# Kernel optimization log

Measured on AMD Instinct MI355X. Metric: run time of the kernel, lower is better.

Reference implementation:

```python
import jax, jax.numpy as jnp
import numpy as np

B, L, H, NH, D, I = 2, 2048, 2048, 16, 128, 8192
EPS = 1e-6
ROPE_BASE = 10000.0


def rms_norm(x, w):
    x32 = x.astype(jnp.float32)
    n = x32 * jax.lax.rsqrt(jnp.mean(x32 * x32, axis=-1, keepdims=True) + EPS)
    return (n * w).astype(x.dtype)


def rope(x, offset):
    # x: [B, L, H, D], non-traditional (half-split) RoPE
    d = x.shape[-1]
    half = d // 2
    inv_freq = 1.0 / (ROPE_BASE ** (jnp.arange(half, dtype=jnp.float32) * 2.0 / d))
    pos = jnp.arange(x.shape[1], dtype=jnp.float32) + offset
    ang = pos[:, None] * inv_freq[None, :]              # [L, half]
    cos = jnp.cos(ang)[None, :, None, :]
    sin = jnp.sin(ang)[None, :, None, :]
    x1, x2 = x[..., :half], x[..., half:]
    out = jnp.concatenate([x1 * cos - x2 * sin, x2 * cos + x1 * sin], axis=-1)
    return out.astype(x.dtype)


def setup_inputs() -> dict:
    key = jax.random.key(0)
    ks = jax.random.split(key, 9)
    s = 0.02
    causal = jnp.where(jnp.tril(jnp.ones((L, L), dtype=bool)), 0.0, -1e9).astype(jnp.float32)
    return {
        "x": jax.random.normal(ks[0], (B, L, H), dtype=jnp.float32),
        "ln1_w": jnp.ones((H,), dtype=jnp.float32),
        "ln2_w": jnp.ones((H,), dtype=jnp.float32),
        "wq": jax.random.normal(ks[1], (H, H), dtype=jnp.float32) * s,
        "wk": jax.random.normal(ks[2], (H, H), dtype=jnp.float32) * s,
        "wv": jax.random.normal(ks[3], (H, H), dtype=jnp.float32) * s,
        "wo": jax.random.normal(ks[4], (H, H), dtype=jnp.float32) * s,
        "w_gate": jax.random.normal(ks[5], (I, H), dtype=jnp.float32) * s,
        "w_up": jax.random.normal(ks[6], (I, H), dtype=jnp.float32) * s,
        "w_down": jax.random.normal(ks[7], (H, I), dtype=jnp.float32) * s,
        "mask": causal,
        "offset": 0,
    }


def reference(x, ln1_w, ln2_w, wq, wk, wv, wo, w_gate, w_up, w_down, mask, offset):
    residual = x
    h = rms_norm(x, ln1_w)
    # QKV projections (torch Linear: y = x @ W.T)
    q = jnp.einsum("ble,oe->blo", h, wq).reshape(B, L, NH, D)
    k = jnp.einsum("ble,oe->blo", h, wk).reshape(B, L, NH, D)
    v = jnp.einsum("ble,oe->blo", h, wv).reshape(B, L, NH, D)
    q = rope(q, offset)
    k = rope(k, offset)
    # [B, NH, L, D]
    q = q.transpose(0, 2, 1, 3)
    k = k.transpose(0, 2, 1, 3)
    v = v.transpose(0, 2, 1, 3)
    scores = jnp.einsum("bhqd,bhkd->bhqk", q.astype(jnp.float32), k.astype(jnp.float32))
    scores = scores / np.sqrt(D).astype(np.float32)
    if mask is not None:
        scores = scores + mask
    probs = jax.nn.softmax(scores, axis=-1).astype(v.dtype)
    attn = jnp.einsum("bhqk,bhkd->bhqd", probs, v)
    attn = attn.transpose(0, 2, 1, 3).reshape(B, L, NH * D)
    h = jnp.einsum("blo,eo->ble", attn, wo)
    x = h + residual
    residual = x
    h = rms_norm(x, ln2_w)
    gate = jax.nn.silu(jnp.einsum("ble,ie->bli", h, w_gate))
    up = jnp.einsum("ble,ie->bli", h, w_up)
    mlp = jnp.einsum("bli,ei->ble", gate * up, w_down)
    return mlp + residual
```

## Files before the change

### kernel.cpp

```cpp
#include <hip/hip_runtime.h>
#include <stdint.h>

#define B_ 2
#define L_ 2048
#define H_ 2048
#define NH_ 16
#define D_ 128
#define I_ 8192
#define M_ (B_*L_)

typedef unsigned short u16;
typedef __attribute__((ext_vector_type(8))) short bf16x8;
typedef __attribute__((ext_vector_type(4))) float f32x4;

__device__ __forceinline__ u16 f2bf(float f) {
  union { float f; uint32_t u; } c; c.f = f;
  return (u16)((c.u + 0x7fffu + ((c.u >> 16) & 1u)) >> 16);
}
__device__ __forceinline__ float bf2f(u16 h) {
  union { uint32_t u; float f; } c; c.u = ((uint32_t)h) << 16;
  return c.f;
}
__device__ __forceinline__ void gload16(const void* g, void* l) {
  __builtin_amdgcn_global_load_lds(
      (__attribute__((address_space(1))) void*)g,
      (__attribute__((address_space(3))) void*)l, 16, 0, 0);
}

__global__ void cvt_w(const float* __restrict__ src, u16* __restrict__ dst, int n4) {
  int i = blockIdx.x * blockDim.x + threadIdx.x;
  if (i >= n4) return;
  float4 v = ((const float4*)src)[i];
  ushort4 o;
  o.x = f2bf(v.x); o.y = f2bf(v.y); o.z = f2bf(v.z); o.w = f2bf(v.w);
  ((ushort4*)dst)[i] = o;
}

__global__ __launch_bounds__(256) void down_reduce(const u16* __restrict__ p0,
                                                   const u16* __restrict__ p1,
                                                   const float* __restrict__ res,
                                                   float* __restrict__ out, int n4) {
  int i = blockIdx.x * blockDim.x + threadIdx.x;
  if (i >= n4) return;
  ushort4 a = ((const ushort4*)p0)[i];
  ushort4 b = ((const ushort4*)p1)[i];
  float4 r = ((const float4*)res)[i];
  float4 o;
  o.x = bf2f(a.x) + bf2f(b.x) + r.x;
  o.y = bf2f(a.y) + bf2f(b.y) + r.y;
  o.z = bf2f(a.z) + bf2f(b.z) + r.z;
  o.w = bf2f(a.w) + bf2f(b.w) + r.w;
  ((float4*)out)[i] = o;
}

__global__ __launch_bounds__(256) void rmsnorm_k(const float* __restrict__ x,
                                                 const float* __restrict__ w,
                                                 u16* __restrict__ out) {
  int row = blockIdx.x;
  int t = threadIdx.x;
  const float4* xr = (const float4*)(x + (size_t)row * H_);
  float4 a = xr[t * 2], b = xr[t * 2 + 1];
  float s = a.x*a.x + a.y*a.y + a.z*a.z + a.w*a.w
          + b.x*b.x + b.y*b.y + b.z*b.z + b.w*b.w;
  for (int m = 1; m < 64; m <<= 1) s += __shfl_xor(s, m);
  __shared__ float sm[4];
  if ((t & 63) == 0) sm[t >> 6] = s;
  __syncthreads();
  float tot = sm[0] + sm[1] + sm[2] + sm[3];
  float rs = rsqrtf(tot / (float)H_ + 1e-6f);
  const float4* wr = (const float4*)w;
  float4 w0 = wr[t * 2], w1 = wr[t * 2 + 1];
  ushort4 o0, o1;
  o0.x = f2bf(a.x * rs * w0.x); o0.y = f2bf(a.y * rs * w0.y);
  o0.z = f2bf(a.z * rs * w0.z); o0.w = f2bf(a.w * rs * w0.w);
  o1.x = f2bf(b.x * rs * w1.x); o1.y = f2bf(b.y * rs * w1.y);
  o1.z = f2bf(b.z * rs * w1.z); o1.w = f2bf(b.w * rs * w1.w);
  ushort4* orow = (ushort4*)(out + (size_t)row * H_);
  orow[t * 2] = o0; orow[t * 2 + 1] = o1;
}

__global__ void rope_tab(float* __restrict__ cosT, float* __restrict__ sinT,
                         const int* __restrict__ offp) {
  int i = blockIdx.x * blockDim.x + threadIdx.x;
  int d = i & 63, l = i >> 6;
  float inv = powf(10000.0f, -(float)d / 64.0f);
  float ang = (float)(l + *offp) * inv;
  cosT[i] = cosf(ang);
  sinT[i] = sinf(ang);
}

__global__ void rope_apply(u16* __restrict__ qk, const float* __restrict__ cosT,
                           const float* __restrict__ sinT) {
  int i = blockIdx.x * blockDim.x + threadIdx.x;
  int d = i & 63;
  size_t row = (size_t)(i >> 6);
  int l = (int)(row & (L_ - 1));
  u16* p = qk + row * D_;
  float x1 = bf2f(p[d]), x2 = bf2f(p[d + 64]);
  float c = cosT[l * 64 + d], s = sinT[l * 64 + d];
  p[d]      = f2bf(x1 * c - x2 * s);
  p[d + 64] = f2bf(x2 * c + x1 * s);
}

__global__ __launch_bounds__(256) void vtrans_k(const u16* __restrict__ v,
                                                u16* __restrict__ vt) {
  __shared__ u16 tile[64][65];
  int l0 = blockIdx.x * 64, d0 = blockIdx.y * 64;
  size_t base = (size_t)blockIdx.z * L_ * D_;
  int t = threadIdx.x;
  int tr = t >> 3, tc = (t & 7) * 8;
  #pragma unroll
  for (int it = 0; it < 2; ++it) {
    int r = tr + it * 32;
    const u16* src = v + base + (size_t)(l0 + r) * D_ + d0 + tc;
    ushort4 u0 = ((const ushort4*)src)[0], u1 = ((const ushort4*)src)[1];
    tile[r][tc + 0] = u0.x; tile[r][tc + 1] = u0.y;
    tile[r][tc + 2] = u0.z; tile[r][tc + 3] = u0.w;
    tile[r][tc + 4] = u1.x; tile[r][tc + 5] = u1.y;
    tile[r][tc + 6] = u1.z; tile[r][tc + 7] = u1.w;
  }
  __syncthreads();
  #pragma unroll
  for (int it = 0; it < 2; ++it) {
    int r = tr + it * 32;
    u16* dst = vt + base + (size_t)(d0 + r) * L_ + l0 + tc;
    ushort4 o0, o1;
    o0.x = tile[tc + 0][r]; o0.y = tile[tc + 1][r];
    o0.z = tile[tc + 2][r]; o0.w = tile[tc + 3][r];
    o1.x = tile[tc + 4][r]; o1.y = tile[tc + 5][r];
    o1.z = tile[tc + 6][r]; o1.w = tile[tc + 7][r];
    ((ushort4*)dst)[0] = o0; ((ushort4*)dst)[1] = o1;
  }
}

#define EPI_SILU 1
#define EPI_MUL 2
#define EPI_PART 4
#define EPI_QKV3 5
#define EPI_GLU 6

template <int EPI>
__global__ __launch_bounds__(512, 2)
void gemm256(const u16* __restrict__ A, const u16* __restrict__ Bw,
             int M, int N, int K, int nk,
             u16* __restrict__ outb, u16* __restrict__ outb2,
             const u16* __restrict__ Bw2) {
  __shared__ __attribute__((aligned(16))) u16 Asm[2][2][8192];
  __shared__ __attribute__((aligned(16))) u16 Bsm[2][2][8192];
  int tid = threadIdx.x;
  int wid = tid >> 6, lane = tid & 63;
  int r16 = lane & 15, g4 = lane >> 4;
  int nwg = gridDim.x, bid = blockIdx.x;
  int q8 = nwg >> 3, r8 = nwg & 7, xcd = bid & 7, loc = bid >> 3;
  int wgall = (xcd < r8 ? xcd * (q8 + 1) : r8 * (q8 + 1) + (xcd - r8) * q8) + loc;
  int nwg_geo = (M >> 8) * ((EPI == EPI_GLU) ? (N >> 7) : (N >> 8));
  int ks = wgall / nwg_geo;
  int wg = wgall % nwg_geo;
  int MX = M >> 8;
  int m0 = (wg % MX) * 256;
  int n0 = (wg / MX) * ((EPI == EPI_GLU) ? 128 : 256);
  const char* Ab = (const char*)(A + (size_t)ks * nk * 64);
  const char* Bb = (const char*)(Bw + (size_t)ks * nk * 64);
  const char* Bb2 = (const char*)Bw2;
  u16* ob = (EPI == EPI_PART && ks) ? outb2 : outb;

  f32x4 acc[2][2][4][2] = {};
  bf16x8 afr[4][2];
  bf16x8 bfr[2][2][2];

  auto STAGE = [&](int kt1, int sel) {
    if (kt1 >= nk) return;
    int buf = kt1 & 1;
    int k0 = kt1 << 6;
    const char* gb; char* lb; int row0;
    if (sel == 0)      { gb = Ab; row0 = m0;       lb = (char*)&Asm[buf][0][0]; }
    else if (sel == 3) { gb = Ab; row0 = m0 + 128; lb = (char*)&Asm[buf][1][0]; }
    else if (sel == 1) { gb = Bb; row0 = n0;       lb = (char*)&Bsm[buf][0][0]; }
    else               { gb = (EPI == EPI_GLU) ? Bb2 : Bb;
                         row0 = (EPI == EPI_GLU) ? n0 : n0 + 128;
                         lb = (char*)&Bsm[buf][1][0]; }
    #pragma unroll
    for (int j = 0; j < 2; ++j) {
      int p = j * 8192 + wid * 1024 + lane * 16;
      int r = p >> 7;
      int cb = (p & 127) ^ ((r & 7) << 4);
      gload16(gb + ((size_t)(row0 + r) * K + k0) * 2 + cb,
              lb + j * 8192 + wid * 1024);
    }
  };

  STAGE(0, 0); STAGE(0, 1); STAGE(0, 2); STAGE(0, 3);

  const int QM[4] = {0, 0, 1, 1};
  const int QN[4] = {0, 1, 1, 0};

  for (int kt = 0; kt < nk; ++kt) {
    int cur = kt & 1;
    #pragma unroll
    for (int ph = 0; ph < 4; ++ph) {
      if (ph < 3) {
        __builtin_amdgcn_sched_barrier(0);
        asm volatile("s_waitcnt vmcnt(4)" ::: "memory");
      }
      __builtin_amdgcn_s_barrier();
      __builtin_amdgcn_sched_barrier(0);
      const int qm = QM[ph], qn = QN[ph];
      if (ph == 0 || ph == 2) {
        const char* Ah = (const char*)&Asm[cur][qm][0];
        #pragma unroll
        for (int mf = 0; mf < 4; ++mf) {
          int R = (wid >> 2) * 64 + mf * 16 + r16;
          int sw = (R & 7) << 4;
          afr[mf][0] = *(const bf16x8*)(Ah + R * 128 + ((g4 * 16) ^ sw));
          afr[mf][1] = *(const bf16x8*)(Ah + R * 128 + ((64 + g4 * 16) ^ sw));
        }
      }
      if (ph == 0 || ph == 1) {
        const char* Bh = (const char*)&Bsm[cur][qn][0];
        #pragma unroll
        for (int nf = 0; nf < 2; ++nf) {
          int R = (wid & 3) * 32 + nf * 16 + r16;
          int sw = (R & 7) << 4;
          bfr[qn][nf][0] = *(const bf16x8*)(Bh + R * 128 + ((g4 * 16) ^ sw));
          bfr[qn][nf][1] = *(const bf16x8*)(Bh + R * 128 + ((64 + g4 * 16) ^ sw));
        }
      }
      STAGE(kt + 1, ph);
      __builtin_amdgcn_s_setprio(1);
      #pragma unroll
      for (int mf = 0; mf < 4; ++mf)
        #pragma unroll
        for (int nf = 0; nf < 2; ++nf)
          #pragma unroll
          for (int kk = 0; kk < 2; ++kk)
            acc[qm][qn][mf][nf] = __builtin_amdgcn_mfma_f32_16x16x32_bf16(
                afr[mf][kk], bfr[qn][nf][kk], acc[qm][qn][mf][nf], 0, 0, 0);
      __builtin_amdgcn_s_setprio(0);
    }
  }
  if (EPI == EPI_GLU) {
    #pragma unroll
    for (int qm = 0; qm < 2; ++qm)
      #pragma unroll
      for (int mf = 0; mf < 4; ++mf)
        #pragma unroll
        for (int nf = 0; nf < 2; ++nf)
          #pragma unroll
          for (int rr = 0; rr < 4; ++rr) {
            int row = m0 + qm * 128 + (wid >> 2) * 64 + mf * 16 + g4 * 4 + rr;
            int col = n0 + (wid & 3) * 32 + nf * 16 + r16;
            float g = acc[qm][0][mf][nf][rr];
            float u = acc[qm][1][mf][nf][rr];
            float sg = g / (1.0f + __expf(-g));
            outb[(size_t)row * N + col] = f2bf(sg * u);
          }
    return;
  }
  #pragma unroll
  for (int qm = 0; qm < 2; ++qm)
    #pragma unroll
    for (int qn = 0; qn < 2; ++qn)
      #pragma unroll
      for (int mf = 0; mf < 4; ++mf)
        #pragma unroll
        for (int nf = 0; nf < 2; ++nf)
          #pragma unroll
          for (int rr = 0; rr < 4; ++rr) {
            int row = m0 + qm * 128 + (wid >> 2) * 64 + mf * 16 + g4 * 4 + rr;
            int col = n0 + qn * 128 + (wid & 3) * 32 + nf * 16 + r16;
            float val = acc[qm][qn][mf][nf][rr];
            if (EPI == EPI_SILU) {
              ob[(size_t)row * N + col] = f2bf(val / (1.0f + __expf(-val)));
            } else if (EPI == EPI_MUL) {
              float g = bf2f(ob[(size_t)row * N + col]);
              ob[(size_t)row * N + col] = f2bf(g * val);
            } else if (EPI == EPI_PART) {
              ob[(size_t)row * N + col] = f2bf(val);
            } else if (EPI == EPI_QKV3) {
              int which = col >> 11, within = col & 2047;
              int hh = within >> 7, d = within & 127;
              int bb = row >> 11, l = row & 2047;
              ob[(size_t)which * M_ * H_ +
                 ((((size_t)bb * NH_ + hh) * L_ + l) << 7) + d] = f2bf(val);
            }
          }
}

__global__ __launch_bounds__(256)
void flash_attn(const u16* __restrict__ q, const u16* __restrict__ k,
                const u16* __restrict__ vt, u16* __restrict__ out) {
  __shared__ __attribute__((aligned(16))) u16 Kt[2][64 * 128];
  __shared__ __attribute__((aligned(16))) u16 Vt[2][128 * 64];
  __shared__ __attribute__((aligned(16))) u16 Pl[4][16 * 64];
  int tid = threadIdx.x, w = tid >> 6, lane = tid & 63;
  int r16 = lane & 15, g4 = lane >> 4;
  int b = blockIdx.z, h = blockIdx.y;
  int qt = gridDim.x - 1 - blockIdx.x;
  int q0 = qt * 64;
  size_t bh = (size_t)b * NH_ + h;
  const char* qb = (const char*)(q + bh * L_ * D_);
  const char* kb = (const char*)(k + bh * L_ * D_);
  const char* vb = (const char*)(vt + bh * D_ * L_);
  int qrow = q0 + w * 16 + r16;
  bf16x8 qf[4];
  #pragma unroll
  for (int c = 0; c < 4; ++c)
    qf[c] = *(const bf16x8*)(qb + ((size_t)qrow * 128 + c * 32 + g4 * 8) * 2);
  f32x4 oacc[8] = {};
  float mrow[4], lsum[4];
  #pragma unroll
  for (int r = 0; r < 4; ++r) { mrow[r] = -3.0e38f; lsum[r] = 0.f; }
  int myq = q0 + w * 16 + g4 * 4;
  int ntiles = qt + 1;
  int rsw = (r16 & 7) << 4;
  const float sc = 0.08838834764831845f;

  auto STAGEKV = [&](int t, int buf) {
    if (t >= ntiles) return;
    int kv0 = t * 64;
    #pragma unroll
    for (int i = 0; i < 4; ++i) {
      int uoff = i * 4096 + w * 1024;
      int lin = uoff + lane * 16;
      int krow = lin >> 8;
      int kcol = (lin & 255) ^ ((krow & 7) << 4);
      gload16(kb + (size_t)(kv0 + krow) * 256 + kcol,
              (char*)&Kt[buf][0] + uoff);
      int vrow = lin >> 7;
      int vcol = (lin & 127) ^ ((vrow & 7) << 4);
      gload16(vb + (size_t)vrow * (L_ * 2) + kv0 * 2 + vcol,
              (char*)&Vt[buf][0] + uoff);
    }
  };

  STAGEKV(0, 0);
  __syncthreads();

  for (int t = 0; t < ntiles; ++t) {
    int buf = t & 1;
    int kv0 = t * 64;
    STAGEKV(t + 1, buf ^ 1);
    const char* Kb = (const char*)&Kt[buf][0];
    const char* Vb = (const char*)&Vt[buf][0];
    f32x4 s[4] = {};
    __builtin_amdgcn_s_setprio(1);
    #pragma unroll
    for (int c = 0; c < 4; ++c) {
      #pragma unroll
      for (int n = 0; n < 4; ++n) {
        bf16x8 kf = *(const bf16x8*)(Kb + (n * 16 + r16) * 256
                                     + ((c * 64 + g4 * 16) ^ rsw));
        s[n] = __builtin_amdgcn_mfma_f32_16x16x32_bf16(qf[c], kf, s[n], 0, 0, 0);
      }
    }
    __builtin_amdgcn_s_setprio(0);
    #pragma unroll
    for (int r = 0; r < 4; ++r) {
      float rm = -3.0e38f;
      #pragma unroll
      for (int n = 0; n < 4; ++n) {
        float v = s[n][r] * sc;
        int kvi = kv0 + n * 16 + r16;
        if (kvi > myq + r) v = -3.0e38f;
        s[n][r] = v;
        rm = fmaxf(rm, v);
      }
      rm = fmaxf(rm, __shfl_xor(rm, 1));
      rm = fmaxf(rm, __shfl_xor(rm, 2));
      rm = fmaxf(rm, __shfl_xor(rm, 4));
      rm = fmaxf(rm, __shfl_xor(rm, 8));
      float mnew = fmaxf(mrow[r], rm);
      float alpha = __expf(mrow[r] - mnew);
      mrow[r] = mnew;
      lsum[r] *= alpha;
      #pragma unroll
      for (int nf = 0; nf < 8; ++nf) oacc[nf][r] *= alpha;
      int prow = g4 * 4 + r;
      int psw = (prow & 7) << 3;
      #pragma unroll
      for (int n = 0; n < 4; ++n) {
        float pv = __expf(s[n][r] - mnew);
        lsum[r] += pv;
        Pl[w][prow * 64 + ((n * 16 + r16) ^ psw)] = f2bf(pv);
      }
    }
    asm volatile("s_waitcnt lgkmcnt(0)" ::: "memory");
    __builtin_amdgcn_sched_barrier(0);
    __builtin_amdgcn_s_setprio(1);
    #pragma unroll
    for (int kc = 0; kc < 2; ++kc) {
      bf16x8 pf = *(const bf16x8*)((const char*)&Pl[w][0] + r16 * 128
                                   + ((kc * 64 + g4 * 16) ^ rsw));
      #pragma unroll
      for (int nf = 0; nf < 8; ++nf) {
        bf16x8 vf = *(const bf16x8*)(Vb + (nf * 16 + r16) * 128
                                     + ((kc * 64 + g4 * 16) ^ rsw));
        oacc[nf] = __builtin_amdgcn_mfma_f32_16x16x32_bf16(pf, vf, oacc[nf], 0, 0, 0);
      }
    }
    __builtin_amdgcn_s_setprio(0);
    __syncthreads();
  }
  #pragma unroll
  for (int r = 0; r < 4; ++r) {
    float l = lsum[r];
    l += __shfl_xor(l, 1); l += __shfl_xor(l, 2);
    l += __shfl_xor(l, 4); l += __shfl_xor(l, 8);
    float inv = 1.0f / l;
    size_t orow = ((size_t)b * L_ + (myq + r)) * H_ + h * D_;
    #pragma unroll
    for (int nf = 0; nf < 8; ++nf)
      out[orow + nf * 16 + r16] = f2bf(oacc[nf][r] * inv);
  }
}

extern "C" void kernel_launch(void* const* d_in, const int* in_sizes, int n_in,
                              void* d_out, int out_size, void* d_ws, size_t ws_size,
                              hipStream_t stream) {
  (void)in_sizes; (void)n_in; (void)out_size;
  const float* x    = (const float*)d_in[0];
  const float* ln1w = (const float*)d_in[1];
  const float* ln2w = (const float*)d_in[2];
  const float* wq   = (const float*)d_in[3];
  const float* wk   = (const float*)d_in[4];
  const float* wv   = (const float*)d_in[5];
  const float* wo   = (const float*)d_in[6];
  const float* wg   = (const float*)d_in[7];
  const float* wu   = (const float*)d_in[8];
  const float* wd   = (const float*)d_in[9];
  const int*   offp = (const int*)d_in[11];
  float* out = (float*)d_out;

  char* p = (char*)d_ws;
  auto alloc = [&](size_t bytes) {
    char* r = p;
    p += (bytes + 255) & ~(size_t)255;
    return r;
  };
  const size_t HH = (size_t)H_ * H_, IH = (size_t)I_ * H_;
  u16* wbuf = (u16*)alloc(IH * 2);
  u16* h1   = (u16*)alloc((size_t)M_ * H_ * 2);
  u16* qb   = (u16*)alloc((size_t)M_ * H_ * 2);
  u16* kb   = (u16*)alloc((size_t)M_ * H_ * 2);
  u16* vb   = (u16*)alloc((size_t)M_ * H_ * 2);
  u16* vtb  = (u16*)alloc((size_t)M_ * H_ * 2);
  u16* attn = (u16*)alloc((size_t)M_ * H_ * 2);
  float* x2 = (float*)alloc((size_t)M_ * H_ * 4);
  float* cosT = (float*)alloc((size_t)L_ * 64 * 4);
  float* sinT = (float*)alloc((size_t)L_ * 64 * 4);
  u16* h2    = h1;
  u16* gateb = qb;
  u16* wu_b = (u16*)alloc(IH * 2);
  bool fused_glu = ((char*)wu_b + IH * 2) <= ((char*)d_ws + ws_size);

  const int nHH4 = (int)(HH / 4), nIH4 = (int)(IH / 4);

  rmsnorm_k<<<M_, 256, 0, stream>>>(x, ln1w, h1);
  rope_tab<<<(L_ * 64) / 256, 256, 0, stream>>>(cosT, sinT, offp);

  cvt_w<<<nHH4 / 256, 256, 0, stream>>>(wq, wbuf, nHH4);
  cvt_w<<<nHH4 / 256, 256, 0, stream>>>(wk, wbuf + HH, nHH4);
  cvt_w<<<nHH4 / 256, 256, 0, stream>>>(wv, wbuf + 2 * HH, nHH4);
  int nwg_qkv = (M_ / 256) * (3 * H_ / 256);
  gemm256<EPI_QKV3><<<nwg_qkv, 512, 0, stream>>>(h1, wbuf, M_, 3 * H_, H_,
                                                 H_ / 64, qb, nullptr, nullptr);

  int nrope = B_ * NH_ * L_ * 64;
  rope_apply<<<nrope / 256, 256, 0, stream>>>(qb, cosT, sinT);
  rope_apply<<<nrope / 256, 256, 0, stream>>>(qb + (size_t)M_ * H_, cosT, sinT);
  vtrans_k<<<dim3(L_ / 64, D_ / 64, B_ * NH_), 256, 0, stream>>>(
      qb + 2 * (size_t)M_ * H_, vtb);

  flash_attn<<<dim3(L_ / 64, NH_, B_), 256, 0, stream>>>(
      qb, qb + (size_t)M_ * H_, vtb, attn);

  cvt_w<<<nHH4 / 256, 256, 0, stream>>>(wo, wbuf, nHH4);
  int nwg_wo = 2 * (M_ / 256) * (H_ / 256);
  gemm256<EPI_PART><<<nwg_wo, 512, 0, stream>>>(attn, wbuf, M_, H_, H_,
                                                H_ / 128, kb, vb, nullptr);
  down_reduce<<<(M_ * H_ / 4) / 256, 256, 0, stream>>>(kb, vb, x, x2,
                                                       M_ * H_ / 4);
  rmsnorm_k<<<M_, 256, 0, stream>>>(x2, ln2w, h2);

  if (fused_glu) {
    cvt_w<<<nIH4 / 256, 256, 0, stream>>>(wg, wbuf, nIH4);
    cvt_w<<<nIH4 / 256, 256, 0, stream>>>(wu, wu_b, nIH4);
    int nwg_glu = (M_ / 256) * (I_ / 128);
    gemm256<EPI_GLU><<<nwg_glu, 512, 0, stream>>>(h2, wbuf, M_, I_, H_,
                                                  H_ / 64, gateb, nullptr, wu_b);
  } else {
    int nwg256 = (M_ / 256) * (I_ / 256);
    cvt_w<<<nIH4 / 256, 256, 0, stream>>>(wg, wbuf, nIH4);
    gemm256<EPI_SILU><<<nwg256, 512, 0, stream>>>(h2, wbuf, M_, I_, H_,
                                                  H_ / 64, gateb, nullptr, nullptr);
    cvt_w<<<nIH4 / 256, 256, 0, stream>>>(wu, wbuf, nIH4);
    gemm256<EPI_MUL><<<nwg256, 512, 0, stream>>>(h2, wbuf, M_, I_, H_,
                                                 H_ / 64, gateb, nullptr, nullptr);
  }

  cvt_w<<<nIH4 / 256, 256, 0, stream>>>(wd, wbuf, nIH4);
  int nwg_dn = 2 * (M_ / 256) * (H_ / 256);
  gemm256<EPI_PART><<<nwg_dn, 512, 0, stream>>>(gateb, wbuf, M_, H_, I_,
                                                I_ / 128, h1, attn, nullptr);
  down_reduce<<<(M_ * H_ / 4) / 256, 256, 0, stream>>>(h1, attn, x2, out,
                                                       M_ * H_ / 4);
}
```

Baseline: 794.7 us.

## Overlap weight conversions with GEMM and attention via extra worker blocks; fuse reduce+rmsnorm

Adds extra thread blocks to the QKV GEMM, flash attention and GLU GEMM launches. These blocks convert the next stages' fp32 weights (gate, o-proj, up, down) to bf16 while the main blocks do compute, which removes the standalone cvt_w launches from the critical path. It also fuses the partial-sum reduction with the second RMSNorm into one kernel. The cost is a larger workspace, with a fallback path when space is short, and some contention for bandwidth and CUs with the main compute.

```diff
diff --git a/kernel.cpp b/kernel.cpp
--- a/kernel.cpp
+++ b/kernel.cpp
@@ -51,6 +51,48 @@
   o.z = bf2f(a.z) + bf2f(b.z) + r.z;
   o.w = bf2f(a.w) + bf2f(b.w) + r.w;
   ((float4*)out)[i] = o;
+}
+
+__global__ __launch_bounds__(256)
+void reduce_rms(const u16* __restrict__ p0, const u16* __restrict__ p1,
+                const float* __restrict__ res, const float* __restrict__ w,
+                float* __restrict__ x2o, u16* __restrict__ h2o) {
+  int row = blockIdx.x, t = threadIdx.x;
+  size_t base = (size_t)row * H_;
+  ushort4 a0 = ((const ushort4*)(p0 + base))[t * 2];
+  ushort4 a1 = ((const ushort4*)(p0 + base))[t * 2 + 1];
+  ushort4 b0 = ((const ushort4*)(p1 + base))[t * 2];
+  ushort4 b1 = ((const ushort4*)(p1 + base))[t * 2 + 1];
+  float4 r0 = ((const float4*)(res + base))[t * 2];
+  float4 r1 = ((const float4*)(res + base))[t * 2 + 1];
+  float4 v0, v1;
+  v0.x = bf2f(a0.x) + bf2f(b0.x) + r0.x;
+  v0.y = bf2f(a0.y) + bf2f(b0.y) + r0.y;
+  v0.z = bf2f(a0.z) + bf2f(b0.z) + r0.z;
+  v0.w = bf2f(a0.w) + bf2f(b0.w) + r0.w;
+  v1.x = bf2f(a1.x) + bf2f(b1.x) + r1.x;
+  v1.y = bf2f(a1.y) + bf2f(b1.y) + r1.y;
+  v1.z = bf2f(a1.z) + bf2f(b1.z) + r1.z;
+  v1.w = bf2f(a1.w) + bf2f(b1.w) + r1.w;
+  ((float4*)(x2o + base))[t * 2] = v0;
+  ((float4*)(x2o + base))[t * 2 + 1] = v1;
+  float s = v0.x*v0.x + v0.y*v0.y + v0.z*v0.z + v0.w*v0.w
+          + v1.x*v1.x + v1.y*v1.y + v1.z*v1.z + v1.w*v1.w;
+  for (int m = 1; m < 64; m <<= 1) s += __shfl_xor(s, m);
+  __shared__ float sm[4];
+  if ((t & 63) == 0) sm[t >> 6] = s;
+  __syncthreads();
+  float tot = sm[0] + sm[1] + sm[2] + sm[3];
+  float rs = rsqrtf(tot / (float)H_ + 1e-6f);
+  const float4* wr = (const float4*)w;
+  float4 w0 = wr[t * 2], w1 = wr[t * 2 + 1];
+  ushort4 o0, o1;
+  o0.x = f2bf(v0.x * rs * w0.x); o0.y = f2bf(v0.y * rs * w0.y);
+  o0.z = f2bf(v0.z * rs * w0.z); o0.w = f2bf(v0.w * rs * w0.w);
+  o1.x = f2bf(v1.x * rs * w1.x); o1.y = f2bf(v1.y * rs * w1.y);
+  o1.z = f2bf(v1.z * rs * w1.z); o1.w = f2bf(v1.w * rs * w1.w);
+  ((ushort4*)(h2o + base))[t * 2] = o0;
+  ((ushort4*)(h2o + base))[t * 2 + 1] = o1;
 }
 
 __global__ __launch_bounds__(256) void rmsnorm_k(const float* __restrict__ x,
@@ -144,7 +186,9 @@
 void gemm256(const u16* __restrict__ A, const u16* __restrict__ Bw,
              int M, int N, int K, int nk,
              u16* __restrict__ outb, u16* __restrict__ outb2,
-             const u16* __restrict__ Bw2) {
+             const u16* __restrict__ Bw2,
+             const float* __restrict__ cv_src, u16* __restrict__ cv_dst,
+             int cv_n4, int gemm_blocks) {
   __shared__ __attribute__((aligned(16))) u16 Asm[2][2][8192];
   __shared__ __attribute__((aligned(16))) u16 Bsm[2][2][8192];
   int tid = threadIdx.x;
@@ -153,6 +197,19 @@
   int nwg = gridDim.x, bid = blockIdx.x;
   int q8 = nwg >> 3, r8 = nwg & 7, xcd = bid & 7, loc = bid >> 3;
   int wgall = (xcd < r8 ? xcd * (q8 + 1) : r8 * (q8 + 1) + (xcd - r8) * q8) + loc;
+  if (wgall >= gemm_blocks) {
+    if (cv_src != nullptr) {
+      int wk = wgall - gemm_blocks;
+      int stride = (nwg - gemm_blocks) * 512;
+      for (int i = wk * 512 + tid; i < cv_n4; i += stride) {
+        float4 v = ((const float4*)cv_src)[i];
+        ushort4 o;
+        o.x = f2bf(v.x); o.y = f2bf(v.y); o.z = f2bf(v.z); o.w = f2bf(v.w);
+        ((ushort4*)cv_dst)[i] = o;
+      }
+    }
+    return;
+  }
   int nwg_geo = (M >> 8) * ((EPI == EPI_GLU) ? (N >> 7) : (N >> 8));
   int ks = wgall / nwg_geo;
   int wg = wgall % nwg_geo;
@@ -288,14 +345,38 @@
 
 __global__ __launch_bounds__(256)
 void flash_attn(const u16* __restrict__ q, const u16* __restrict__ k,
-                const u16* __restrict__ vt, u16* __restrict__ out) {
+                const u16* __restrict__ vt, u16* __restrict__ out,
+                const float* __restrict__ cvA, u16* __restrict__ dstA, int n4A,
+                const float* __restrict__ cvB, u16* __restrict__ dstB, int n4B) {
   __shared__ __attribute__((aligned(16))) u16 Kt[2][64 * 128];
   __shared__ __attribute__((aligned(16))) u16 Vt[2][128 * 64];
   __shared__ __attribute__((aligned(16))) u16 Pl[4][16 * 64];
+  if (blockIdx.x >= 32) {
+    int wk = (blockIdx.x - 32) + 4 * (blockIdx.y + 16 * blockIdx.z);
+    int t = threadIdx.x;
+    if (wk < 32) {
+      if (cvA != nullptr)
+        for (int i = wk * 256 + t; i < n4A; i += 32 * 256) {
+          float4 v = ((const float4*)cvA)[i];
+          ushort4 o;
+          o.x = f2bf(v.x); o.y = f2bf(v.y); o.z = f2bf(v.z); o.w = f2bf(v.w);
+          ((ushort4*)dstA)[i] = o;
+        }
+    } else {
+      if (cvB != nullptr)
+        for (int i = (wk - 32) * 256 + t; i < n4B; i += 96 * 256) {
+          float4 v = ((const float4*)cvB)[i];
+          ushort4 o;
+          o.x = f2bf(v.x); o.y = f2bf(v.y); o.z = f2bf(v.z); o.w = f2bf(v.w);
+          ((ushort4*)dstB)[i] = o;
+        }
+    }
+    return;
+  }
   int tid = threadIdx.x, w = tid >> 6, lane = tid & 63;
   int r16 = lane & 15, g4 = lane >> 4;
   int b = blockIdx.z, h = blockIdx.y;
-  int qt = gridDim.x - 1 - blockIdx.x;
+  int qt = 31 - blockIdx.x;
   int q0 = qt * 64;
   size_t bh = (size_t)b * NH_ + h;
   const char* qb = (const char*)(q + bh * L_ * D_);
@@ -438,7 +519,6 @@
     return r;
   };
   const size_t HH = (size_t)H_ * H_, IH = (size_t)I_ * H_;
-  u16* wbuf = (u16*)alloc(IH * 2);
   u16* h1   = (u16*)alloc((size_t)M_ * H_ * 2);
   u16* qb   = (u16*)alloc((size_t)M_ * H_ * 2);
   u16* kb   = (u16*)alloc((size_t)M_ * H_ * 2);
@@ -448,12 +528,28 @@
   float* x2 = (float*)alloc((size_t)M_ * H_ * 4);
   float* cosT = (float*)alloc((size_t)L_ * 64 * 4);
   float* sinT = (float*)alloc((size_t)L_ * 64 * 4);
+  u16* wbuf = (u16*)alloc(3 * HH * 2);
   u16* h2    = h1;
   u16* gateb = qb;
-  u16* wu_b = (u16*)alloc(IH * 2);
-  bool fused_glu = ((char*)wu_b + IH * 2) <= ((char*)d_ws + ws_size);
+  size_t used = (size_t)(p - (char*)d_ws);
+  size_t need_fast = 3 * ((IH * 2 + 255) & ~(size_t)255) + ((HH * 2 + 255) & ~(size_t)255);
+  bool fast = (used + need_fast) <= ws_size;
+  u16 *wg_b = nullptr, *wu_b = nullptr, *wd_b = nullptr, *wo_b = nullptr;
+  u16 *wbig = nullptr, *wu_m = nullptr;
+  bool fused_glu_m = false;
+  if (fast) {
+    wg_b = (u16*)alloc(IH * 2);
+    wu_b = (u16*)alloc(IH * 2);
+    wd_b = (u16*)alloc(IH * 2);
+    wo_b = (u16*)alloc(HH * 2);
+  } else {
+    wbig = (u16*)alloc(IH * 2);
+    fused_glu_m = ((size_t)(p - (char*)d_ws) + IH * 2) <= ws_size;
+    if (fused_glu_m) wu_m = (u16*)alloc(IH * 2);
+  }
 
   const int nHH4 = (int)(HH / 4), nIH4 = (int)(IH / 4);
+  const int MH4 = M_ * H_ / 4;
 
   rmsnorm_k<<<M_, 256, 0, stream>>>(x, ln1w, h1);
   rope_tab<<<(L_ * 64) / 256, 256, 0, stream>>>(cosT, sinT, offp);
@@ -461,47 +557,66 @@
   cvt_w<<<nHH4 / 256, 256, 0, stream>>>(wq, wbuf, nHH4);
   cvt_w<<<nHH4 / 256, 256, 0, stream>>>(wk, wbuf + HH, nHH4);
   cvt_w<<<nHH4 / 256, 256, 0, stream>>>(wv, wbuf + 2 * HH, nHH4);
-  int nwg_qkv = (M_ / 256) * (3 * H_ / 256);
-  gemm256<EPI_QKV3><<<nwg_qkv, 512, 0, stream>>>(h1, wbuf, M_, 3 * H_, H_,
-                                                 H_ / 64, qb, nullptr, nullptr);
-
-  int nrope = B_ * NH_ * L_ * 64;
-  rope_apply<<<nrope / 256, 256, 0, stream>>>(qb, cosT, sinT);
-  rope_apply<<<nrope / 256, 256, 0, stream>>>(qb + (size_t)M_ * H_, cosT, sinT);
-  vtrans_k<<<dim3(L_ / 64, D_ / 64, B_ * NH_), 256, 0, stream>>>(
-      qb + 2 * (size_t)M_ * H_, vtb);
-
-  flash_attn<<<dim3(L_ / 64, NH_, B_), 256, 0, stream>>>(
-      qb, qb + (size_t)M_ * H_, vtb, attn);
-
-  cvt_w<<<nHH4 / 256, 256, 0, stream>>>(wo, wbuf, nHH4);
-  int nwg_wo = 2 * (M_ / 256) * (H_ / 256);
-  gemm256<EPI_PART><<<nwg_wo, 512, 0, stream>>>(attn, wbuf, M_, H_, H_,
-                                                H_ / 128, kb, vb, nullptr);
-  down_reduce<<<(M_ * H_ / 4) / 256, 256, 0, stream>>>(kb, vb, x, x2,
-                                                       M_ * H_ / 4);
-  rmsnorm_k<<<M_, 256, 0, stream>>>(x2, ln2w, h2);
-
-  if (fused_glu) {
-    cvt_w<<<nIH4 / 256, 256, 0, stream>>>(wg, wbuf, nIH4);
-    cvt_w<<<nIH4 / 256, 256, 0, stream>>>(wu, wu_b, nIH4);
-    int nwg_glu = (M_ / 256) * (I_ / 128);
-    gemm256<EPI_GLU><<<nwg_glu, 512, 0, stream>>>(h2, wbuf, M_, I_, H_,
-                                                  H_ / 64, gateb, nullptr, wu_b);
+
+  if (fast) {
+    gemm256<EPI_QKV3><<<512, 512, 0, stream>>>(h1, wbuf, M_, 3 * H_, H_,
+        H_ / 64, qb, nullptr, nullptr, wg, wg_b, nIH4, 384);
+
+    int nrope = B_ * NH_ * L_ * 64;
+    rope_apply<<<nrope / 256, 256, 0, stream>>>(qb, cosT, sinT);
+    rope_apply<<<nrope / 256, 256, 0, stream>>>(qb + (size_t)M_ * H_, cosT, sinT);
+    vtrans_k<<<dim3(L_ / 64, D_ / 64, B_ * NH_), 256, 0, stream>>>(
+        qb + 2 * (size_t)M_ * H_, vtb);
+
+    flash_attn<<<dim3(36, NH_, B_), 256, 0, stream>>>(
+        qb, qb + (size_t)M_ * H_, vtb, attn, wo, wo_b, nHH4, wu, wu_b, nIH4);
+
+    gemm256<EPI_PART><<<256, 512, 0, stream>>>(attn, wo_b, M_, H_, H_,
+        H_ / 128, kb, vb, nullptr, nullptr, nullptr, 0, 256);
+    reduce_rms<<<M_, 256, 0, stream>>>(kb, vb, x, ln2w, x2, h2);
+
+    gemm256<EPI_GLU><<<1280, 512, 0, stream>>>(h2, wg_b, M_, I_, H_,
+        H_ / 64, gateb, nullptr, wu_b, wd, wd_b, nIH4, 1024);
+
+    gemm256<EPI_PART><<<256, 512, 0, stream>>>(gateb, wd_b, M_, H_, I_,
+        I_ / 128, h1, attn, nullptr, nullptr, nullptr, 0, 256);
+    down_reduce<<<MH4 / 256, 256, 0, stream>>>(h1, attn, x2, out, MH4);
   } else {
-    int nwg256 = (M_ / 256) * (I_ / 256);
-    cvt_w<<<nIH4 / 256, 256, 0, stream>>>(wg, wbuf, nIH4);
-    gemm256<EPI_SILU><<<nwg256, 512, 0, stream>>>(h2, wbuf, M_, I_, H_,
-                                                  H_ / 64, gateb, nullptr, nullptr);
-    cvt_w<<<nIH4 / 256, 256, 0, stream>>>(wu, wbuf, nIH4);
-    gemm256<EPI_MUL><<<nwg256, 512, 0, stream>>>(h2, wbuf, M_, I_, H_,
-                                                 H_ / 64, gateb, nullptr, nullptr);
-  }
-
-  cvt_w<<<nIH4 / 256, 256, 0, stream>>>(wd, wbuf, nIH4);
-  int nwg_dn = 2 * (M_ / 256) * (H_ / 256);
-  gemm256<EPI_PART><<<nwg_dn, 512, 0, stream>>>(gateb, wbuf, M_, H_, I_,
-                                                I_ / 128, h1, attn, nullptr);
-  down_reduce<<<(M_ * H_ / 4) / 256, 256, 0, stream>>>(h1, attn, x2, out,
-                                                       M_ * H_ / 4);
-}
+    gemm256<EPI_QKV3><<<384, 512, 0, stream>>>(h1, wbuf, M_, 3 * H_, H_,
+        H_ / 64, qb, nullptr, nullptr, nullptr, nullptr, 0, 384);
+
+    int nrope = B_ * NH_ * L_ * 64;
+    rope_apply<<<nrope / 256, 256, 0, stream>>>(qb, cosT, sinT);
+    rope_apply<<<nrope / 256, 256, 0, stream>>>(qb + (size_t)M_ * H_, cosT, sinT);
+    vtrans_k<<<dim3(L_ / 64, D_ / 64, B_ * NH_), 256, 0, stream>>>(
+        qb + 2 * (size_t)M_ * H_, vtb);
+
+    flash_attn<<<dim3(32, NH_, B_), 256, 0, stream>>>(
+        qb, qb + (size_t)M_ * H_, vtb, attn,
+        nullptr, nullptr, 0, nullptr, nullptr, 0);
+
+    cvt_w<<<nHH4 / 256, 256, 0, stream>>>(wo, wbig, nHH4);
+    gemm256<EPI_PART><<<256, 512, 0, stream>>>(attn, wbig, M_, H_, H_,
+        H_ / 128, kb, vb, nullptr, nullptr, nullptr, 0, 256);
+    reduce_rms<<<M_, 256, 0, stream>>>(kb, vb, x, ln2w, x2, h2);
+
+    if (fused_glu_m) {
+      cvt_w<<<nIH4 / 256, 256, 0, stream>>>(wg, wbig, nIH4);
+      cvt_w<<<nIH4 / 256, 256, 0, stream>>>(wu, wu_m, nIH4);
+      gemm256<EPI_GLU><<<1024, 512, 0, stream>>>(h2, wbig, M_, I_, H_,
+          H_ / 64, gateb, nullptr, wu_m, nullptr, nullptr, 0, 1024);
+    } else {
+      cvt_w<<<nIH4 / 256, 256, 0, stream>>>(wg, wbig, nIH4);
+      gemm256<EPI_SILU><<<512, 512, 0, stream>>>(h2, wbig, M_, I_, H_,
+          H_ / 64, gateb, nullptr, nullptr, nullptr, nullptr, 0, 512);
+      cvt_w<<<nIH4 / 256, 256, 0, stream>>>(wu, wbig, nIH4);
+      gemm256<EPI_MUL><<<512, 512, 0, stream>>>(h2, wbig, M_, I_, H_,
+          H_ / 64, gateb, nullptr, nullptr, nullptr, nullptr, 0, 512);
+    }
+
+    cvt_w<<<nIH4 / 256, 256, 0, stream>>>(wd, wbig, nIH4);
+    gemm256<EPI_PART><<<256, 512, 0, stream>>>(gateb, wbig, M_, H_, I_,
+        I_ / 128, h1, attn, nullptr, nullptr, nullptr, 0, 256);
+    down_reduce<<<MH4 / 256, 256, 0, stream>>>(h1, attn, x2, out, MH4);
+  }
+}
```

Result: slower. 846.7 us (+6.5%).
